# Kernel optimization log

Hardware: AMD Instinct MI355X
Metric: run time of the kernel (lower is better)

Reference implementation:

```python
import jax, jax.numpy as jnp
import numpy as np

NUM_CLASSES = 100000
FEATURE_LEN = 256
BATCH = 16384
DECAY = 0.99


def setup_inputs() -> dict:
    key = jax.random.key(0)
    k1, k2, k3 = jax.random.split(key, 3)
    batch_feature = jax.random.normal(k1, (BATCH, FEATURE_LEN), dtype=jnp.float32)
    batch_label = jax.random.randint(k2, (BATCH,), 0, NUM_CLASSES, dtype=jnp.int64)
    center_feature = jax.random.normal(k3, (NUM_CLASSES, FEATURE_LEN), dtype=jnp.float32)
    return {"batch_feature": batch_feature, "batch_label": batch_label,
            "center_feature": center_feature}


def reference(batch_feature, batch_label, center_feature):
    # scatter-mean of features per class (single pass, replaces per-class python loop)
    sums = jax.ops.segment_sum(batch_feature, batch_label, num_segments=NUM_CLASSES)  # [C, F]
    counts = jax.ops.segment_sum(jnp.ones((batch_feature.shape[0],), batch_feature.dtype),
                                 batch_label, num_segments=NUM_CLASSES)  # [C]
    mean_per_class = sums / jnp.maximum(counts, 1.0)[:, None]
    present = (counts > 0)[:, None]
    # EMA update only for classes present in the batch
    new_center = jnp.where(present,
                           DECAY * center_feature + (1.0 - DECAY) * mean_per_class,
                           center_feature)
    # gather updated centers per sample and take MSE (mean reduction, as nn.MSELoss)
    gathered = new_center[batch_label]  # [B, F]
    loss = jnp.mean((batch_feature - gathered) ** 2)
    return loss
```

## Files before the change

### kernel.cpp

```cpp
#include <hip/hip_runtime.h>


#define NUM_CLASSES 100000
#define FEAT 256
#define BATCH 16384
#define DECAYF 0.99f

static constexpr int BLOCKS_UNIQ = BATCH / 4;
static constexpr int BLOCKS_DUP  = 8192 / 4;
static constexpr int NPART       = BLOCKS_UNIQ + BLOCKS_DUP;

static constexpr size_t WS_COUNTS = 0;
static constexpr size_t WS_NDUP   = 100000;
static constexpr size_t WS_PART   = 100032;
static constexpr size_t WS_WORK   = 106176;
static constexpr size_t WS_HEAD   = 114368;
static constexpr size_t WS_NEXT   = 214368;

__global__ __launch_bounds__(256) void count_chain(
    const int* __restrict__ label, float* __restrict__ counts,
    int* __restrict__ head, int* __restrict__ next,
    float* __restrict__ ndup, int* __restrict__ work) {
  int s = blockIdx.x * 256 + threadIdx.x;
  int l = label[s];
  next[s] = atomicExch(&head[l], s);
  float old = atomicAdd(&counts[l], 1.0f);
  if (old == 1.0f) {
    float w = atomicAdd(ndup, 1.0f);
    work[(int)(w + 0.5f)] = l;
  }
}

__global__ __launch_bounds__(256) void loss_fused(
    const float* __restrict__ x, const int* __restrict__ label,
    const float* __restrict__ centers, const float* __restrict__ counts,
    const int* __restrict__ head, const int* __restrict__ next,
    const float* __restrict__ ndup, const int* __restrict__ work,
    float* __restrict__ partial) {
  int grp = threadIdx.x >> 6;
  int t = threadIdx.x & 63;
  float p = 0.0f;

  if (blockIdx.x < BLOCKS_UNIQ) {
    int s = blockIdx.x * 4 + grp;
    int l = label[s];
    if (counts[l] < 1.5f) {
      float4 xv = reinterpret_cast<const float4*>(x + (size_t)s * FEAT)[t];
      float4 cv = reinterpret_cast<const float4*>(centers + (size_t)l * FEAT)[t];
      float dx = xv.x - cv.x, dy = xv.y - cv.y, dz = xv.z - cv.z, dw = xv.w - cv.w;
      p = (DECAYF * DECAYF) * (dx * dx + dy * dy + dz * dz + dw * dw);
    }
  } else {
    int g = (blockIdx.x - BLOCKS_UNIQ) * 4 + grp;
    int nd = (int)(ndup[0] + 0.5f);
    if (g < nd) {
      int c = work[g];
      float n = counts[c];
      float4 sum = make_float4(0.f, 0.f, 0.f, 0.f);
      float sq = 0.0f;
      int idx = head[c];
      while (idx >= 0) {
        float4 v = reinterpret_cast<const float4*>(x + (size_t)idx * FEAT)[t];
        sum.x += v.x; sum.y += v.y; sum.z += v.z; sum.w += v.w;
        sq += v.x * v.x + v.y * v.y + v.z * v.z + v.w * v.w;
        idx = next[idx];
      }
      float4 cv = reinterpret_cast<const float4*>(centers + (size_t)c * FEAT)[t];
      float inv = 1.0f / n;
      float mx = sum.x * inv, my = sum.y * inv, mz = sum.z * inv, mw = sum.w * inv;
      float ncx = DECAYF * cv.x + 0.01f * mx;
      float ncy = DECAYF * cv.y + 0.01f * my;
      float ncz = DECAYF * cv.z + 0.01f * mz;
      float ncw = DECAYF * cv.w + 0.01f * mw;
      float ncnc = ncx * ncx + ncy * ncy + ncz * ncz + ncw * ncw;
      float mnc  = mx * ncx + my * ncy + mz * ncz + mw * ncw;
      p = sq + n * (ncnc - 2.0f * mnc);
    }
  }

  #pragma unroll
  for (int off = 32; off > 0; off >>= 1) p += __shfl_down(p, off, 64);
  __shared__ float wsum[4];
  if (t == 0) wsum[grp] = p;
  __syncthreads();
  if (threadIdx.x == 0)
    partial[blockIdx.x] = wsum[0] + wsum[1] + wsum[2] + wsum[3];
}

__global__ __launch_bounds__(256) void finalize(
    const float* __restrict__ partial, float* __restrict__ out) {
  float v = 0.0f;
  for (int i = threadIdx.x; i < NPART; i += 256) v += partial[i];
  #pragma unroll
  for (int off = 32; off > 0; off >>= 1) v += __shfl_down(v, off, 64);
  __shared__ float wsum[4];
  if ((threadIdx.x & 63) == 0) wsum[threadIdx.x >> 6] = v;
  __syncthreads();
  if (threadIdx.x == 0)
    out[0] = (wsum[0] + wsum[1] + wsum[2] + wsum[3]) *
             (1.0f / (float)((size_t)BATCH * FEAT));
}

extern "C" void kernel_launch(void* const* d_in, const int* in_sizes, int n_in,
                              void* d_out, int out_size, void* d_ws, size_t ws_size,
                              hipStream_t stream) {
  const float* x = (const float*)d_in[0];
  const int* label = (const int*)d_in[1];
  const float* centers = (const float*)d_in[2];
  float* ws = (float*)d_ws;
  float* counts = ws + WS_COUNTS;
  float* ndup = ws + WS_NDUP;
  float* partial = ws + WS_PART;
  int* work = (int*)(ws + WS_WORK);
  int* head = (int*)(ws + WS_HEAD);
  int* next = (int*)(ws + WS_NEXT);
  float* out = (float*)d_out;

  dim3 block(256);
  count_chain<<<dim3(BATCH / 256), block, 0, stream>>>(label, counts, head, next,
                                                       ndup, work);
  loss_fused<<<dim3(NPART), block, 0, stream>>>(
      x, label, centers, counts, head, next, ndup, work, partial);
  finalize<<<1, block, 0, stream>>>(partial, out);
}
```

Baseline: 158.8 us.

## Assign duplicate-class reduction to the chain-head sample instead of a work list

Drops the separate duplicate work list and its global atomic counter. Each sample's wavefront now handles its own row, and when its class appears more than once, the wave whose sample is the linked-list head walks the chain and computes that class's contribution. This removes the extra 2048 mostly idle blocks and the serialized atomic on a single counter. In exchange, chain walks now run inside the main grid, and x and center rows are loaded unconditionally even for waves that contribute nothing.

```diff
diff --git a/kernel.cpp b/kernel.cpp
--- a/kernel.cpp
+++ b/kernel.cpp
@@ -6,76 +6,59 @@
 #define BATCH 16384
 #define DECAYF 0.99f
 
-static constexpr int BLOCKS_UNIQ = BATCH / 4;
-static constexpr int BLOCKS_DUP  = 8192 / 4;
-static constexpr int NPART       = BLOCKS_UNIQ + BLOCKS_DUP;
+static constexpr int NPART = BATCH / 4;
 
 static constexpr size_t WS_COUNTS = 0;
-static constexpr size_t WS_NDUP   = 100000;
-static constexpr size_t WS_PART   = 100032;
-static constexpr size_t WS_WORK   = 106176;
-static constexpr size_t WS_HEAD   = 114368;
-static constexpr size_t WS_NEXT   = 214368;
+static constexpr size_t WS_PART   = 100000;
+static constexpr size_t WS_HEAD   = 104096;
+static constexpr size_t WS_NEXT   = 204096;
 
 __global__ __launch_bounds__(256) void count_chain(
     const int* __restrict__ label, float* __restrict__ counts,
-    int* __restrict__ head, int* __restrict__ next,
-    float* __restrict__ ndup, int* __restrict__ work) {
+    int* __restrict__ head, int* __restrict__ next) {
   int s = blockIdx.x * 256 + threadIdx.x;
   int l = label[s];
   next[s] = atomicExch(&head[l], s);
-  float old = atomicAdd(&counts[l], 1.0f);
-  if (old == 1.0f) {
-    float w = atomicAdd(ndup, 1.0f);
-    work[(int)(w + 0.5f)] = l;
-  }
+  atomicAdd(&counts[l], 1.0f);
 }
 
 __global__ __launch_bounds__(256) void loss_fused(
     const float* __restrict__ x, const int* __restrict__ label,
     const float* __restrict__ centers, const float* __restrict__ counts,
     const int* __restrict__ head, const int* __restrict__ next,
-    const float* __restrict__ ndup, const int* __restrict__ work,
     float* __restrict__ partial) {
   int grp = threadIdx.x >> 6;
   int t = threadIdx.x & 63;
+  int s = blockIdx.x * 4 + grp;
+  int l = label[s];
+  float4 xv = reinterpret_cast<const float4*>(x + (size_t)s * FEAT)[t];
+  float4 cv = reinterpret_cast<const float4*>(centers + (size_t)l * FEAT)[t];
+  float n = counts[l];
+  int h = head[l];
+
   float p = 0.0f;
-
-  if (blockIdx.x < BLOCKS_UNIQ) {
-    int s = blockIdx.x * 4 + grp;
-    int l = label[s];
-    if (counts[l] < 1.5f) {
-      float4 xv = reinterpret_cast<const float4*>(x + (size_t)s * FEAT)[t];
-      float4 cv = reinterpret_cast<const float4*>(centers + (size_t)l * FEAT)[t];
-      float dx = xv.x - cv.x, dy = xv.y - cv.y, dz = xv.z - cv.z, dw = xv.w - cv.w;
-      p = (DECAYF * DECAYF) * (dx * dx + dy * dy + dz * dz + dw * dw);
+  if (n < 1.5f) {
+    float dx = xv.x - cv.x, dy = xv.y - cv.y, dz = xv.z - cv.z, dw = xv.w - cv.w;
+    p = (DECAYF * DECAYF) * (dx * dx + dy * dy + dz * dz + dw * dw);
+  } else if (h == s) {
+    float4 sum = xv;
+    float sq = xv.x * xv.x + xv.y * xv.y + xv.z * xv.z + xv.w * xv.w;
+    int idx = next[s];
+    while (idx >= 0) {
+      float4 v = reinterpret_cast<const float4*>(x + (size_t)idx * FEAT)[t];
+      sum.x += v.x; sum.y += v.y; sum.z += v.z; sum.w += v.w;
+      sq += v.x * v.x + v.y * v.y + v.z * v.z + v.w * v.w;
+      idx = next[idx];
     }
-  } else {
-    int g = (blockIdx.x - BLOCKS_UNIQ) * 4 + grp;
-    int nd = (int)(ndup[0] + 0.5f);
-    if (g < nd) {
-      int c = work[g];
-      float n = counts[c];
-      float4 sum = make_float4(0.f, 0.f, 0.f, 0.f);
-      float sq = 0.0f;
-      int idx = head[c];
-      while (idx >= 0) {
-        float4 v = reinterpret_cast<const float4*>(x + (size_t)idx * FEAT)[t];
-        sum.x += v.x; sum.y += v.y; sum.z += v.z; sum.w += v.w;
-        sq += v.x * v.x + v.y * v.y + v.z * v.z + v.w * v.w;
-        idx = next[idx];
-      }
-      float4 cv = reinterpret_cast<const float4*>(centers + (size_t)c * FEAT)[t];
-      float inv = 1.0f / n;
-      float mx = sum.x * inv, my = sum.y * inv, mz = sum.z * inv, mw = sum.w * inv;
-      float ncx = DECAYF * cv.x + 0.01f * mx;
-      float ncy = DECAYF * cv.y + 0.01f * my;
-      float ncz = DECAYF * cv.z + 0.01f * mz;
-      float ncw = DECAYF * cv.w + 0.01f * mw;
-      float ncnc = ncx * ncx + ncy * ncy + ncz * ncz + ncw * ncw;
-      float mnc  = mx * ncx + my * ncy + mz * ncz + mw * ncw;
-      p = sq + n * (ncnc - 2.0f * mnc);
-    }
+    float inv = 1.0f / n;
+    float mx = sum.x * inv, my = sum.y * inv, mz = sum.z * inv, mw = sum.w * inv;
+    float ncx = DECAYF * cv.x + 0.01f * mx;
+    float ncy = DECAYF * cv.y + 0.01f * my;
+    float ncz = DECAYF * cv.z + 0.01f * mz;
+    float ncw = DECAYF * cv.w + 0.01f * mw;
+    float ncnc = ncx * ncx + ncy * ncy + ncz * ncz + ncw * ncw;
+    float mnc  = mx * ncx + my * ncy + mz * ncz + mw * ncw;
+    p = sq + n * (ncnc - 2.0f * mnc);
   }
 
   #pragma unroll
@@ -109,17 +92,14 @@
   const float* centers = (const float*)d_in[2];
   float* ws = (float*)d_ws;
   float* counts = ws + WS_COUNTS;
-  float* ndup = ws + WS_NDUP;
   float* partial = ws + WS_PART;
-  int* work = (int*)(ws + WS_WORK);
   int* head = (int*)(ws + WS_HEAD);
   int* next = (int*)(ws + WS_NEXT);
   float* out = (float*)d_out;
 
   dim3 block(256);
-  count_chain<<<dim3(BATCH / 256), block, 0, stream>>>(label, counts, head, next,
-                                                       ndup, work);
+  count_chain<<<dim3(BATCH / 256), block, 0, stream>>>(label, counts, head, next);
   loss_fused<<<dim3(NPART), block, 0, stream>>>(
-      x, label, centers, counts, head, next, ndup, work, partial);
+      x, label, centers, counts, head, next, partial);
   finalize<<<1, block, 0, stream>>>(partial, out);
 }
```

New measurement: 152.8 us. 1.04x faster.
